# Kernel optimization log

Measured on AMD Instinct MI355X. Metric: run time of the kernel, lower is better.

## Reference

```python
import jax, jax.numpy as jnp
import numpy as np

D_MODEL = 1024
N_HEADS = 16
D_HEAD = D_MODEL // N_HEADS

def setup_inputs() -> dict:
    key = jax.random.key(0)
    kx, kq, kk, kv, ko = jax.random.split(key, 5)
    s = 1.0 / np.sqrt(D_MODEL)
    return {
        "x": jax.random.normal(kx, (4, 2048, D_MODEL), dtype=jnp.float32),
        "W_q": jax.random.normal(kq, (D_MODEL, D_MODEL), dtype=jnp.float32) * s,
        "W_k": jax.random.normal(kk, (D_MODEL, D_MODEL), dtype=jnp.float32) * s,
        "W_v": jax.random.normal(kv, (D_MODEL, D_MODEL), dtype=jnp.float32) * s,
        "W_o": jax.random.normal(ko, (D_MODEL, D_MODEL), dtype=jnp.float32) * s,
    }

def reference(x, W_q, W_k, W_v, W_o):
    B, L, _ = x.shape
    def heads(h):  # (B,L,D) -> (B,H,L,d_head)
        return h.reshape(B, L, N_HEADS, D_HEAD).transpose(0, 2, 1, 3)
    # nn.Linear: y = x @ W.T
    q = heads(x @ W_q.T)
    k = heads(x @ W_k.T)
    v = heads(x @ W_v.T)
    scores = jnp.einsum('bhqd,bhkd->bhqk', q, k) / jnp.sqrt(jnp.float32(D_HEAD))
    attn = jax.nn.softmax(scores, axis=-1)
    ctx = jnp.einsum('bhqk,bhkd->bhqd', attn, v)
    ctx = ctx.transpose(0, 2, 1, 3).reshape(B, L, D_MODEL)
    return ctx @ W_o.T
```

## Files before the change

### kernel.cpp

```cpp
#include <hip/hip_runtime.h>
#include <hip/hip_fp16.h>

typedef _Float16 f16;
typedef _Float16 f16x4 __attribute__((ext_vector_type(4)));
typedef _Float16 f16x8 __attribute__((ext_vector_type(8)));
typedef float f32x4 __attribute__((ext_vector_type(4)));

#define NHEADS 16
#define DHEAD 64
#define DM 1024
#define BATCH 4
#define SEQ 2048
#define MTOT (BATCH*SEQ)

__device__ inline void gload_lds16(const void* g, void* l) {
  __builtin_amdgcn_global_load_lds(
      (const __attribute__((address_space(1))) void*)g,
      (__attribute__((address_space(3))) void*)l, 16, 0, 0);
}

__global__ __launch_bounds__(256) void cvt_f32_f16_k(const float* __restrict__ s,
                                                     f16* __restrict__ d, int n) {
  int i = (blockIdx.x * 256 + threadIdx.x) * 8;
  if (i + 8 <= n) {
    float4 a = *reinterpret_cast<const float4*>(s + i);
    float4 b = *reinterpret_cast<const float4*>(s + i + 4);
    f16x8 h = {(f16)a.x,(f16)a.y,(f16)a.z,(f16)a.w,(f16)b.x,(f16)b.y,(f16)b.z,(f16)b.w};
    *reinterpret_cast<f16x8*>(d + i) = h;
  } else {
    for (int j = i; j < n; ++j) d[j] = (f16)s[j];
  }
}

__global__ __launch_bounds__(256) void cvt_w4_k(const float* __restrict__ w0,
                                                const float* __restrict__ w1,
                                                const float* __restrict__ w2,
                                                const float* __restrict__ w3,
                                                f16* __restrict__ d) {
  int which = blockIdx.x >> 9;
  const float* s = which == 0 ? w0 : which == 1 ? w1 : which == 2 ? w2 : w3;
  int off = ((blockIdx.x & 511) * 256 + threadIdx.x) * 8;
  float4 a = *reinterpret_cast<const float4*>(s + off);
  float4 b = *reinterpret_cast<const float4*>(s + off + 4);
  f16x8 h = {(f16)a.x,(f16)a.y,(f16)a.z,(f16)a.w,(f16)b.x,(f16)b.y,(f16)b.z,(f16)b.w};
  *reinterpret_cast<f16x8*>(d + (size_t)which * DM * DM + off) = h;
}

template <int MODE>
__device__ void gemm_nt_body(const f16* __restrict__ A, const f16* __restrict__ Bw,
                             void* __restrict__ outp, int n0, float oscale,
                             f16* Ah, f16* Bh) {
  const int tx = threadIdx.x;
  const int wave = tx >> 6, lane = tx & 63;
  const int m0 = blockIdx.y * 128;
  const int wm = (wave >> 1) * 64, wn = (wave & 1) * 64;

  f32x4 acc[4][4];
#pragma unroll
  for (int i = 0; i < 4; ++i)
#pragma unroll
    for (int j = 0; j < 4; ++j) acc[i][j] = {0.f, 0.f, 0.f, 0.f};

  const int srow = lane >> 2;
  const int scol = (lane & 3) * 8;

  for (int k0 = 0; k0 < DM; k0 += 32) {
    __syncthreads();
#pragma unroll
    for (int i = 0; i < 2; ++i) {
      int chunk = wave * 2 + i;
      gload_lds16(A  + (size_t)(m0 + chunk * 16 + srow) * DM + k0 + scol, Ah + chunk * 512);
      gload_lds16(Bw + (size_t)(n0 + chunk * 16 + srow) * DM + k0 + scol, Bh + chunk * 512);
    }
    __syncthreads();

    f16x8 af[4], bf[4];
#pragma unroll
    for (int i = 0; i < 4; ++i)
      af[i] = *reinterpret_cast<const f16x8*>(Ah + (wm + i * 16 + (lane & 15)) * 32 + (lane >> 4) * 8);
#pragma unroll
    for (int j = 0; j < 4; ++j)
      bf[j] = *reinterpret_cast<const f16x8*>(Bh + (wn + j * 16 + (lane & 15)) * 32 + (lane >> 4) * 8);
#pragma unroll
    for (int i = 0; i < 4; ++i)
#pragma unroll
      for (int j = 0; j < 4; ++j)
        acc[i][j] = __builtin_amdgcn_mfma_f32_16x16x32_f16(af[i], bf[j], acc[i][j], 0, 0, 0);
  }

  const int r0 = (lane >> 4) * 4, c0 = lane & 15;
#pragma unroll
  for (int i = 0; i < 4; ++i)
#pragma unroll
    for (int j = 0; j < 4; ++j)
#pragma unroll
      for (int r = 0; r < 4; ++r) {
        int gm = m0 + wm + i * 16 + r0 + r;
        int gn = n0 + wn + j * 16 + c0;
        float v = acc[i][j][r] * oscale;
        if (MODE == 2) {
          ((float*)outp)[(size_t)gm * DM + gn] = v;
        } else {
          int b = gm >> 11, l = gm & 2047, h = gn >> 6, d = gn & 63;
          size_t idx = (MODE == 0)
            ? (((size_t)(b * NHEADS + h) * SEQ + l) * DHEAD + d)
            : (((size_t)(b * NHEADS + h) * DHEAD + d) * SEQ + l);
          ((f16*)outp)[idx] = (f16)v;
        }
      }
}

__global__ __launch_bounds__(256) void gemm_qkv(const f16* __restrict__ xh,
                                                const f16* __restrict__ Wf,
                                                f16* __restrict__ Qb,
                                                f16* __restrict__ Kb,
                                                f16* __restrict__ VTb,
                                                float qscale) {
  __shared__ f16 Ah[128 * 32];
  __shared__ f16 Bh[128 * 32];
  int which = blockIdx.x >> 3;
  int n0 = (blockIdx.x & 7) * 128;
  const f16* Bw = Wf + (size_t)which * DM * DM;
  if (which == 0)      gemm_nt_body<0>(xh, Bw, Qb,  n0, qscale, Ah, Bh);
  else if (which == 1) gemm_nt_body<0>(xh, Bw, Kb,  n0, 1.0f,  Ah, Bh);
  else                 gemm_nt_body<1>(xh, Bw, VTb, n0, 1.0f,  Ah, Bh);
}

__global__ __launch_bounds__(256) void gemm_out(const f16* __restrict__ A,
                                                const f16* __restrict__ Bw,
                                                float* __restrict__ outp) {
  __shared__ f16 Ah[128 * 32];
  __shared__ f16 Bh[128 * 32];
  gemm_nt_body<2>(A, Bw, outp, blockIdx.x * 128, 1.0f, Ah, Bh);
}

__global__ __launch_bounds__(256, 3) void attn_k(const f16* __restrict__ Q,
                                                 const f16* __restrict__ Kg,
                                                 const f16* __restrict__ VT,
                                                 f16* __restrict__ ctx) {
  __shared__ f16 Kt[2][64 * 64];
  __shared__ f16 Vt[2][64 * 64];
  __shared__ f16 Pl[4][16 * 64];
  const int tx = threadIdx.x, wave = tx >> 6, lane = tx & 63;
  const int g = lane >> 4, qi = lane & 15;
  const int qsw = qi & 7;
  const int bh = blockIdx.y;
  const int q0 = blockIdx.x * 128;
  const f16* Qb = Q  + (size_t)bh * SEQ * DHEAD;
  const f16* Kb = Kg + (size_t)bh * SEQ * DHEAD;
  const f16* Vb = VT + (size_t)bh * DHEAD * SEQ;

  const int gi0 = wave * 128 + lane, gi1 = gi0 + 64;
  const int r0s = gi0 >> 3, sc0 = (((gi0 & 7) ^ (r0s & 7))) * 8;
  const int r1s = gi1 >> 3, sc1 = (((gi1 & 7) ^ (r1s & 7))) * 8;

  auto stage = [&](int buf, int k0) {
    gload_lds16(Kb + (size_t)(k0 + r0s) * DHEAD + sc0, &Kt[buf][(size_t)(wave * 128) * 8]);
    gload_lds16(Kb + (size_t)(k0 + r1s) * DHEAD + sc1, &Kt[buf][(size_t)(wave * 128 + 64) * 8]);
    gload_lds16(Vb + (size_t)r0s * SEQ + k0 + sc0,     &Vt[buf][(size_t)(wave * 128) * 8]);
    gload_lds16(Vb + (size_t)r1s * SEQ + k0 + sc1,     &Vt[buf][(size_t)(wave * 128 + 64) * 8]);
  };

  f16x8 qa[2][2];
#pragma unroll
  for (int hf = 0; hf < 2; ++hf)
#pragma unroll
    for (int ks = 0; ks < 2; ++ks)
      qa[hf][ks] = *reinterpret_cast<const f16x8*>(
          Qb + (size_t)(q0 + wave * 32 + hf * 16 + qi) * DHEAD + g * 8 + ks * 32);

  const f16x8 ones = {(f16)1, (f16)1, (f16)1, (f16)1, (f16)1, (f16)1, (f16)1, (f16)1};
  f32x4 oacc[2][4], lacc[2];
#pragma unroll
  for (int hf = 0; hf < 2; ++hf) {
    lacc[hf] = {0.f, 0.f, 0.f, 0.f};
#pragma unroll
    for (int n = 0; n < 4; ++n) oacc[hf][n] = {0.f, 0.f, 0.f, 0.f};
  }
  float mrun[2] = {-1e30f, -1e30f};

  auto compute = [&](const f16* Kc, const f16* Vc) {
    f16x8 kb[2][4];
#pragma unroll
    for (int ks = 0; ks < 2; ++ks)
#pragma unroll
      for (int t = 0; t < 4; ++t)
        kb[ks][t] = *reinterpret_cast<const f16x8*>(Kc + ((t * 16 + qi) * 8 + ((g + 4 * ks) ^ qsw)) * 8);

    f32x4 st[2][4];
    __builtin_amdgcn_s_setprio(1);
#pragma unroll
    for (int hf = 0; hf < 2; ++hf)
#pragma unroll
      for (int t = 0; t < 4; ++t) {
        f32x4 a = __builtin_amdgcn_mfma_f32_16x16x32_f16(kb[0][t], qa[hf][0], {0.f,0.f,0.f,0.f}, 0, 0, 0);
        st[hf][t] = __builtin_amdgcn_mfma_f32_16x16x32_f16(kb[1][t], qa[hf][1], a, 0, 0, 0);
      }
    __builtin_amdgcn_s_setprio(0);

    f16x8 vb[2][4];
#pragma unroll
    for (int ks = 0; ks < 2; ++ks)
#pragma unroll
      for (int n = 0; n < 4; ++n)
        vb[ks][n] = *reinterpret_cast<const f16x8*>(Vc + ((n * 16 + qi) * 8 + ((g + 4 * ks) ^ qsw)) * 8);

#pragma unroll
    for (int hf = 0; hf < 2; ++hf) {
      float a0 = fmaxf(fmaxf(st[hf][0][0], st[hf][0][1]), fmaxf(st[hf][0][2], st[hf][0][3]));
      float a1 = fmaxf(fmaxf(st[hf][1][0], st[hf][1][1]), fmaxf(st[hf][1][2], st[hf][1][3]));
      float a2 = fmaxf(fmaxf(st[hf][2][0], st[hf][2][1]), fmaxf(st[hf][2][2], st[hf][2][3]));
      float a3 = fmaxf(fmaxf(st[hf][3][0], st[hf][3][1]), fmaxf(st[hf][3][2], st[hf][3][3]));
      float mx = fmaxf(fmaxf(a0, a1), fmaxf(a2, a3));
      mx = fmaxf(mx, __shfl_xor(mx, 16));
      mx = fmaxf(mx, __shfl_xor(mx, 32));

      if (!__all(mx <= mrun[hf] + 8.f)) {
        float mnew = fmaxf(mrun[hf], mx);
        float scl = __builtin_amdgcn_exp2f(mrun[hf] - mnew);
#pragma unroll
        for (int n = 0; n < 4; ++n)
#pragma unroll
          for (int r = 0; r < 4; ++r) oacc[hf][n][r] *= scl;
#pragma unroll
        for (int r = 0; r < 4; ++r) lacc[hf][r] *= scl;
        mrun[hf] = mnew;
      }

#pragma unroll
      for (int t = 0; t < 4; ++t) {
        f16x4 h = {(f16)__builtin_amdgcn_exp2f(st[hf][t][0] - mrun[hf]),
                   (f16)__builtin_amdgcn_exp2f(st[hf][t][1] - mrun[hf]),
                   (f16)__builtin_amdgcn_exp2f(st[hf][t][2] - mrun[hf]),
                   (f16)__builtin_amdgcn_exp2f(st[hf][t][3] - mrun[hf])};
        *reinterpret_cast<f16x4*>(
            &Pl[wave][qi * 64 + (((2 * t + (g >> 1)) ^ qsw) * 8) + 4 * (g & 1)]) = h;
      }
      f16x8 pb[2];
#pragma unroll
      for (int ks = 0; ks < 2; ++ks)
        pb[ks] = *reinterpret_cast<const f16x8*>(&Pl[wave][qi * 64 + (((g + 4 * ks) ^ qsw) * 8)]);

      __builtin_amdgcn_s_setprio(1);
#pragma unroll
      for (int ks = 0; ks < 2; ++ks) {
        lacc[hf] = __builtin_amdgcn_mfma_f32_16x16x32_f16(ones, pb[ks], lacc[hf], 0, 0, 0);
#pragma unroll
        for (int n = 0; n < 4; ++n)
          oacc[hf][n] = __builtin_amdgcn_mfma_f32_16x16x32_f16(vb[ks][n], pb[ks], oacc[hf][n], 0, 0, 0);
      }
      __builtin_amdgcn_s_setprio(0);
    }
  };

  stage(0, 0);
  __syncthreads();
  for (int tt = 0; tt < 32; tt += 2) {
    stage(1, (tt + 1) * 64);
    compute(Kt[0], Vt[0]);
    __syncthreads();
    if (tt + 2 < 32) stage(0, (tt + 2) * 64);
    compute(Kt[1], Vt[1]);
    __syncthreads();
  }

  const int b = bh >> 4, hd = bh & 15;
#pragma unroll
  for (int hf = 0; hf < 2; ++hf) {
    const float inv = 1.0f / lacc[hf][0];
    const int q = q0 + wave * 32 + hf * 16 + qi;
#pragma unroll
    for (int n = 0; n < 4; ++n) {
      f16x4 o = {(f16)(oacc[hf][n][0] * inv), (f16)(oacc[hf][n][1] * inv),
                 (f16)(oacc[hf][n][2] * inv), (f16)(oacc[hf][n][3] * inv)};
      *reinterpret_cast<f16x4*>(ctx + ((size_t)b * SEQ + q) * DM + hd * DHEAD + n * 16 + 4 * g) = o;
    }
  }
}

extern "C" void kernel_launch(void* const* d_in, const int* in_sizes, int n_in,
                              void* d_out, int out_size, void* d_ws, size_t ws_size,
                              hipStream_t stream) {
  (void)in_sizes; (void)n_in; (void)out_size; (void)ws_size;
  const float* x  = (const float*)d_in[0];
  const float* Wq = (const float*)d_in[1];
  const float* Wk = (const float*)d_in[2];
  const float* Wv = (const float*)d_in[3];
  const float* Wo = (const float*)d_in[4];

  char* ws = (char*)d_ws;
  const size_t SZ_X = (size_t)MTOT * DM * sizeof(f16);
  const size_t SZ_W = (size_t)DM * DM * sizeof(f16);
  f16* xh  = (f16*)(ws);
  f16* wfh = (f16*)(ws + SZ_X);
  f16* woh = (f16*)(ws + SZ_X + 3 * SZ_W);
  f16* Qb  = (f16*)(ws + 1 * SZ_X + 4 * SZ_W);
  f16* Kb  = (f16*)(ws + 2 * SZ_X + 4 * SZ_W);
  f16* VTb = (f16*)(ws + 3 * SZ_X + 4 * SZ_W);
  f16* ctx = xh;

  const int nx = MTOT * DM;
  const float QSCALE = 0.125f * 1.44269504088896f;

  cvt_f32_f16_k<<<nx / 2048, 256, 0, stream>>>(x, xh, nx);
  cvt_w4_k<<<2048, 256, 0, stream>>>(Wq, Wk, Wv, Wo, wfh);

  gemm_qkv<<<dim3(24, MTOT / 128), 256, 0, stream>>>(xh, wfh, Qb, Kb, VTb, QSCALE);

  attn_k<<<dim3(SEQ / 128, BATCH * NHEADS), 256, 0, stream>>>(Qb, Kb, VTb, ctx);

  gemm_out<<<dim3(DM / 128, MTOT / 128), 256, 0, stream>>>(ctx, woh, (float*)d_out);
}
```

Measured before the change: 228.6 us.

## Switch attention to 32x32x16 MFMA with register-only P via permlane32 swap

The attention kernel moves from 16x16x32 MFMA tiles to 32x32x16 tiles, so each wave handles 32 query rows in a single accumulator set. The P matrix is packed to f16 with cvt_pkrtz and rearranged across half-waves with v_permlane32_swap, which removes the per-wave LDS round trip for P and its LDS buffer. The row-max reduction uses max3 trees and needs one fewer cross-lane shuffle, and launch bounds rise to 4 blocks per CU. The risks are higher register pressure from 16-wide accumulators, possible spills at the higher occupancy target, and round-toward-zero conversion of P.

```diff
diff --git a/kernel.cpp b/kernel.cpp
--- a/kernel.cpp
+++ b/kernel.cpp
@@ -2,9 +2,11 @@
 #include <hip/hip_fp16.h>
 
 typedef _Float16 f16;
+typedef _Float16 f16x2 __attribute__((ext_vector_type(2)));
 typedef _Float16 f16x4 __attribute__((ext_vector_type(4)));
 typedef _Float16 f16x8 __attribute__((ext_vector_type(8)));
 typedef float f32x4 __attribute__((ext_vector_type(4)));
+typedef float f32x16 __attribute__((ext_vector_type(16)));
 
 #define NHEADS 16
 #define DHEAD 64
@@ -17,6 +19,15 @@
   __builtin_amdgcn_global_load_lds(
       (const __attribute__((address_space(1))) void*)g,
       (__attribute__((address_space(3))) void*)l, 16, 0, 0);
+}
+
+__device__ inline float max3f(float a, float b, float c) {
+  return fmaxf(fmaxf(a, b), c);
+}
+
+__device__ inline unsigned pkrtz(float a, float b) {
+  auto h = __builtin_amdgcn_cvt_pkrtz(a, b);
+  unsigned u; __builtin_memcpy(&u, &h, 4); return u;
 }
 
 __global__ __launch_bounds__(256) void cvt_f32_f16_k(const float* __restrict__ s,
@@ -134,16 +145,14 @@
   gemm_nt_body<2>(A, Bw, outp, blockIdx.x * 128, 1.0f, Ah, Bh);
 }
 
-__global__ __launch_bounds__(256, 3) void attn_k(const f16* __restrict__ Q,
+__global__ __launch_bounds__(256, 4) void attn_k(const f16* __restrict__ Q,
                                                  const f16* __restrict__ Kg,
                                                  const f16* __restrict__ VT,
                                                  f16* __restrict__ ctx) {
   __shared__ f16 Kt[2][64 * 64];
   __shared__ f16 Vt[2][64 * 64];
-  __shared__ f16 Pl[4][16 * 64];
   const int tx = threadIdx.x, wave = tx >> 6, lane = tx & 63;
-  const int g = lane >> 4, qi = lane & 15;
-  const int qsw = qi & 7;
+  const int m = lane & 31, hi = lane >> 5, m7 = m & 7;
   const int bh = blockIdx.y;
   const int q0 = blockIdx.x * 128;
   const f16* Qb = Q  + (size_t)bh * SEQ * DHEAD;
@@ -161,96 +170,86 @@
     gload_lds16(Vb + (size_t)r1s * SEQ + k0 + sc1,     &Vt[buf][(size_t)(wave * 128 + 64) * 8]);
   };
 
-  f16x8 qa[2][2];
-#pragma unroll
-  for (int hf = 0; hf < 2; ++hf)
-#pragma unroll
-    for (int ks = 0; ks < 2; ++ks)
-      qa[hf][ks] = *reinterpret_cast<const f16x8*>(
-          Qb + (size_t)(q0 + wave * 32 + hf * 16 + qi) * DHEAD + g * 8 + ks * 32);
+  f16x8 qb[4];
+#pragma unroll
+  for (int s = 0; s < 4; ++s)
+    qb[s] = *reinterpret_cast<const f16x8*>(
+        Qb + (size_t)(q0 + wave * 32 + m) * DHEAD + s * 16 + hi * 8);
 
   const f16x8 ones = {(f16)1, (f16)1, (f16)1, (f16)1, (f16)1, (f16)1, (f16)1, (f16)1};
-  f32x4 oacc[2][4], lacc[2];
-#pragma unroll
-  for (int hf = 0; hf < 2; ++hf) {
-    lacc[hf] = {0.f, 0.f, 0.f, 0.f};
-#pragma unroll
-    for (int n = 0; n < 4; ++n) oacc[hf][n] = {0.f, 0.f, 0.f, 0.f};
-  }
-  float mrun[2] = {-1e30f, -1e30f};
+  f32x16 oacc[2], lacc;
+#pragma unroll
+  for (int r = 0; r < 16; ++r) { oacc[0][r] = 0.f; oacc[1][r] = 0.f; lacc[r] = 0.f; }
+  float mrun = -1e30f;
 
   auto compute = [&](const f16* Kc, const f16* Vc) {
-    f16x8 kb[2][4];
-#pragma unroll
-    for (int ks = 0; ks < 2; ++ks)
-#pragma unroll
-      for (int t = 0; t < 4; ++t)
-        kb[ks][t] = *reinterpret_cast<const f16x8*>(Kc + ((t * 16 + qi) * 8 + ((g + 4 * ks) ^ qsw)) * 8);
-
-    f32x4 st[2][4];
+    f32x16 st[2];
     __builtin_amdgcn_s_setprio(1);
 #pragma unroll
-    for (int hf = 0; hf < 2; ++hf)
-#pragma unroll
-      for (int t = 0; t < 4; ++t) {
-        f32x4 a = __builtin_amdgcn_mfma_f32_16x16x32_f16(kb[0][t], qa[hf][0], {0.f,0.f,0.f,0.f}, 0, 0, 0);
-        st[hf][t] = __builtin_amdgcn_mfma_f32_16x16x32_f16(kb[1][t], qa[hf][1], a, 0, 0, 0);
+    for (int kt = 0; kt < 2; ++kt) {
+      f32x16 a;
+#pragma unroll
+      for (int r = 0; r < 16; ++r) a[r] = 0.f;
+#pragma unroll
+      for (int s = 0; s < 4; ++s) {
+        f16x8 ka = *reinterpret_cast<const f16x8*>(
+            Kc + ((kt * 32 + m) * 8 + ((2 * s + hi) ^ m7)) * 8);
+        a = __builtin_amdgcn_mfma_f32_32x32x16_f16(ka, qb[s], a, 0, 0, 0);
       }
+      st[kt] = a;
+    }
     __builtin_amdgcn_s_setprio(0);
 
-    f16x8 vb[2][4];
-#pragma unroll
-    for (int ks = 0; ks < 2; ++ks)
-#pragma unroll
-      for (int n = 0; n < 4; ++n)
-        vb[ks][n] = *reinterpret_cast<const f16x8*>(Vc + ((n * 16 + qi) * 8 + ((g + 4 * ks) ^ qsw)) * 8);
-
-#pragma unroll
-    for (int hf = 0; hf < 2; ++hf) {
-      float a0 = fmaxf(fmaxf(st[hf][0][0], st[hf][0][1]), fmaxf(st[hf][0][2], st[hf][0][3]));
-      float a1 = fmaxf(fmaxf(st[hf][1][0], st[hf][1][1]), fmaxf(st[hf][1][2], st[hf][1][3]));
-      float a2 = fmaxf(fmaxf(st[hf][2][0], st[hf][2][1]), fmaxf(st[hf][2][2], st[hf][2][3]));
-      float a3 = fmaxf(fmaxf(st[hf][3][0], st[hf][3][1]), fmaxf(st[hf][3][2], st[hf][3][3]));
-      float mx = fmaxf(fmaxf(a0, a1), fmaxf(a2, a3));
-      mx = fmaxf(mx, __shfl_xor(mx, 16));
-      mx = fmaxf(mx, __shfl_xor(mx, 32));
-
-      if (!__all(mx <= mrun[hf] + 8.f)) {
-        float mnew = fmaxf(mrun[hf], mx);
-        float scl = __builtin_amdgcn_exp2f(mrun[hf] - mnew);
-#pragma unroll
-        for (int n = 0; n < 4; ++n)
-#pragma unroll
-          for (int r = 0; r < 4; ++r) oacc[hf][n][r] *= scl;
-#pragma unroll
-        for (int r = 0; r < 4; ++r) lacc[hf][r] *= scl;
-        mrun[hf] = mnew;
+    float a0 = max3f(st[0][0], st[0][1], st[0][2]);
+    float a1 = max3f(st[0][3], st[0][4], st[0][5]);
+    float a2 = max3f(st[0][6], st[0][7], st[0][8]);
+    float a3 = max3f(st[0][9], st[0][10], st[0][11]);
+    float a4 = max3f(st[0][12], st[0][13], st[0][14]);
+    float a5 = max3f(st[0][15], st[1][0], st[1][1]);
+    float a6 = max3f(st[1][2], st[1][3], st[1][4]);
+    float a7 = max3f(st[1][5], st[1][6], st[1][7]);
+    float a8 = max3f(st[1][8], st[1][9], st[1][10]);
+    float a9 = max3f(st[1][11], st[1][12], st[1][13]);
+    float b0 = max3f(a0, a1, a2), b1 = max3f(a3, a4, a5);
+    float b2 = max3f(a6, a7, a8), b3 = max3f(a9, st[1][14], st[1][15]);
+    float mx = fmaxf(fmaxf(b0, b1), fmaxf(b2, b3));
+    mx = fmaxf(mx, __shfl_xor(mx, 32));
+
+    if (!__all(mx <= mrun + 8.f)) {
+      float mnew = fmaxf(mrun, mx);
+      float scl = __builtin_amdgcn_exp2f(mrun - mnew);
+#pragma unroll
+      for (int r = 0; r < 16; ++r) { oacc[0][r] *= scl; oacc[1][r] *= scl; lacc[r] *= scl; }
+      mrun = mnew;
+    }
+
+    unsigned pk[2][8];
+#pragma unroll
+    for (int kt = 0; kt < 2; ++kt)
+#pragma unroll
+      for (int j = 0; j < 8; ++j)
+        pk[kt][j] = pkrtz(__builtin_amdgcn_exp2f(st[kt][2 * j] - mrun),
+                          __builtin_amdgcn_exp2f(st[kt][2 * j + 1] - mrun));
+
+    __builtin_amdgcn_s_setprio(1);
+#pragma unroll
+    for (int c = 0; c < 4; ++c) {
+      const int kt = c >> 1, c1 = c & 1;
+      unsigned w0 = pk[kt][4 * c1 + 0], w1 = pk[kt][4 * c1 + 1];
+      unsigned w2 = pk[kt][4 * c1 + 2], w3 = pk[kt][4 * c1 + 3];
+      asm("v_permlane32_swap_b32 %0, %1" : "+v"(w0), "+v"(w2));
+      asm("v_permlane32_swap_b32 %0, %1" : "+v"(w1), "+v"(w3));
+      union { unsigned u[4]; f16x8 h; } pu;
+      pu.u[0] = w0; pu.u[1] = w1; pu.u[2] = w2; pu.u[3] = w3;
+      lacc = __builtin_amdgcn_mfma_f32_32x32x16_f16(ones, pu.h, lacc, 0, 0, 0);
+#pragma unroll
+      for (int dt = 0; dt < 2; ++dt) {
+        f16x8 va = *reinterpret_cast<const f16x8*>(
+            Vc + ((dt * 32 + m) * 8 + ((2 * c + hi) ^ m7)) * 8);
+        oacc[dt] = __builtin_amdgcn_mfma_f32_32x32x16_f16(va, pu.h, oacc[dt], 0, 0, 0);
       }
-
-#pragma unroll
-      for (int t = 0; t < 4; ++t) {
-        f16x4 h = {(f16)__builtin_amdgcn_exp2f(st[hf][t][0] - mrun[hf]),
-                   (f16)__builtin_amdgcn_exp2f(st[hf][t][1] - mrun[hf]),
-                   (f16)__builtin_amdgcn_exp2f(st[hf][t][2] - mrun[hf]),
-                   (f16)__builtin_amdgcn_exp2f(st[hf][t][3] - mrun[hf])};
-        *reinterpret_cast<f16x4*>(
-            &Pl[wave][qi * 64 + (((2 * t + (g >> 1)) ^ qsw) * 8) + 4 * (g & 1)]) = h;
-      }
-      f16x8 pb[2];
-#pragma unroll
-      for (int ks = 0; ks < 2; ++ks)
-        pb[ks] = *reinterpret_cast<const f16x8*>(&Pl[wave][qi * 64 + (((g + 4 * ks) ^ qsw) * 8)]);
-
-      __builtin_amdgcn_s_setprio(1);
-#pragma unroll
-      for (int ks = 0; ks < 2; ++ks) {
-        lacc[hf] = __builtin_amdgcn_mfma_f32_16x16x32_f16(ones, pb[ks], lacc[hf], 0, 0, 0);
-#pragma unroll
-        for (int n = 0; n < 4; ++n)
-          oacc[hf][n] = __builtin_amdgcn_mfma_f32_16x16x32_f16(vb[ks][n], pb[ks], oacc[hf][n], 0, 0, 0);
-      }
-      __builtin_amdgcn_s_setprio(0);
-    }
+    }
+    __builtin_amdgcn_s_setprio(0);
   };
 
   stage(0, 0);
@@ -265,17 +264,17 @@
   }
 
   const int b = bh >> 4, hd = bh & 15;
-#pragma unroll
-  for (int hf = 0; hf < 2; ++hf) {
-    const float inv = 1.0f / lacc[hf][0];
-    const int q = q0 + wave * 32 + hf * 16 + qi;
-#pragma unroll
-    for (int n = 0; n < 4; ++n) {
-      f16x4 o = {(f16)(oacc[hf][n][0] * inv), (f16)(oacc[hf][n][1] * inv),
-                 (f16)(oacc[hf][n][2] * inv), (f16)(oacc[hf][n][3] * inv)};
-      *reinterpret_cast<f16x4*>(ctx + ((size_t)b * SEQ + q) * DM + hd * DHEAD + n * 16 + 4 * g) = o;
-    }
-  }
+  const float inv = 1.0f / lacc[0];
+  const int q = q0 + wave * 32 + m;
+  f16* obase = ctx + ((size_t)b * SEQ + q) * DM + hd * DHEAD;
+#pragma unroll
+  for (int dt = 0; dt < 2; ++dt)
+#pragma unroll
+    for (int t = 0; t < 4; ++t) {
+      f16x4 o = {(f16)(oacc[dt][4 * t + 0] * inv), (f16)(oacc[dt][4 * t + 1] * inv),
+                 (f16)(oacc[dt][4 * t + 2] * inv), (f16)(oacc[dt][4 * t + 3] * inv)};
+      *reinterpret_cast<f16x4*>(obase + dt * 32 + t * 8 + 4 * hi) = o;
+    }
 }
 
 extern "C" void kernel_launch(void* const* d_in, const int* in_sizes, int n_in,
```

New measurement: 225.3 us. Within noise of the previous version (-1.5%).
